# Performance work log

Hardware: AMD Instinct MI355X
Metric: run time of the kernel (lower is better)

## Reference

```python
import jax, jax.numpy as jnp
import numpy as np
import math

B, T, C, H = 2, 1024, 1024, 16
D = C // H


def setup_inputs() -> dict:
    key = jax.random.key(0)
    ks = jax.random.split(key, 7)
    scale = 1.0 / math.sqrt(C)
    q = jax.random.normal(ks[0], (B, T, C), dtype=jnp.float32)
    k = jax.random.normal(ks[1], (B, T, C), dtype=jnp.float32)
    v = jax.random.normal(ks[2], (B, T, C), dtype=jnp.float32)
    # causal mask, True = masked out (matches create_causal_mask)
    mask = jnp.triu(jnp.ones((T, T), dtype=bool), k=1)[None, None]
    Wk = jax.random.normal(ks[3], (C, C), dtype=jnp.float32) * scale
    bk = jax.random.normal(ks[4], (C,), dtype=jnp.float32) * scale
    Wc = jax.random.normal(ks[5], (C, C), dtype=jnp.float32) * scale
    bc = jax.random.normal(ks[6], (C,), dtype=jnp.float32) * scale
    return {"q": q, "k": k, "v": v, "mask": mask, "Wk": Wk, "bk": bk, "Wc": Wc, "bc": bc}


def reference(q, k, v, mask, Wk, bk, Wc, bc):
    # NOTE: original module uses self.k_attn for ALL of q, k, v (q_attn/v_attn unused).
    qB, qT, qC = q.shape
    kT = k.shape[1]
    qp = (q @ Wk.T + bk).reshape(qB, qT, H, D).transpose(0, 2, 1, 3)  # [B,H,Tq,D]
    kp = (k @ Wk.T + bk).reshape(qB, kT, H, D).transpose(0, 2, 1, 3)  # [B,H,Tk,D]
    vp = (v @ Wk.T + bk).reshape(qB, kT, H, D).transpose(0, 2, 1, 3)  # [B,H,Tk,D]
    att = jnp.einsum('bhqd,bhkd->bhqk', qp, kp) * (1.0 / math.sqrt(D))
    att = jnp.where(mask, -jnp.inf, att)
    att = jax.nn.softmax(att, axis=-1)
    y = jnp.einsum('bhqk,bhkd->bhqd', att, vp)
    y = y.transpose(0, 2, 1, 3).reshape(qB, qT, qC)
    return y @ Wc.T + bc
```

## Files before the change

### kernel.cpp

```cpp
#include <hip/hip_runtime.h>

#define T_DIM 1024
#define C_DIM 1024
#define H_DIM 16
#define D_DIM 64
#define KD    1024

typedef short  short8  __attribute__((ext_vector_type(8)));
typedef short  short4v __attribute__((ext_vector_type(4)));
typedef float  f32x4   __attribute__((ext_vector_type(4)));

__device__ __forceinline__ float bf2f(short s) {
  return __uint_as_float(((unsigned)(unsigned short)s) << 16);
}
__device__ __forceinline__ short f2bf(float f) {
  unsigned u = __float_as_uint(f);
  u += 0x7fffu + ((u >> 16) & 1u);
  return (short)(u >> 16);
}
__device__ __forceinline__ unsigned pk2(float lo, float hi) {
  return ((unsigned)(unsigned short)f2bf(lo)) | (((unsigned)(unsigned short)f2bf(hi)) << 16);
}

__device__ __forceinline__ short8 ldfrag(const void* p, size_t off, int isf32) {
  if (isf32) {
    const float* q = (const float*)p + off;
    f32x4 lo = *(const f32x4*)q;
    f32x4 hi = *(const f32x4*)(q + 4);
    short8 r;
#pragma unroll
    for (int j = 0; j < 4; ++j) { r[j] = f2bf(lo[j]); r[j + 4] = f2bf(hi[j]); }
    return r;
  }
  return *(const short8*)((const short*)p + off);
}
__device__ __forceinline__ float ldbias(const void* b, int i, int isf32) {
  return isf32 ? ((const float*)b)[i] : bf2f(((const short*)b)[i]);
}

__device__ __forceinline__ int detect_f32_inblock(const unsigned* w, int lane) {
  int c = 0;
#pragma unroll
  for (int i = 0; i < 4; ++i) {
    unsigned e = (w[lane * 4 + i] >> 7) & 0xffu;
    c += (e >= 110u && e <= 135u) ? 1 : 0;
  }
#pragma unroll
  for (int off = 32; off; off >>= 1) c += __shfl_xor(c, off);
  return (c < 128) ? 1 : 0;
}

#define SZE  ((size_t)2 * T_DIM * C_DIM)
#define QN   ((size_t)2097152)
#define WN   ((size_t)1048576)
#define BN   ((size_t)1024)
#define CVT_TOT (3 * QN + 2 * WN + 2 * BN)

__global__ __launch_bounds__(256) void cvt_k(const void* __restrict__ q,
                                             const void* __restrict__ k,
                                             const void* __restrict__ v,
                                             const void* __restrict__ wk,
                                             const void* __restrict__ wc,
                                             const void* __restrict__ bk,
                                             const void* __restrict__ bc,
                                             short* __restrict__ dst)
{
  const int lane = threadIdx.x & 63;
  const int f = detect_f32_inblock((const unsigned*)q, lane);

  const size_t idx = (size_t)blockIdx.x * 1024 + threadIdx.x * 4;
  if (idx >= CVT_TOT) return;
  const void* src;
  size_t loc;
  if      (idx <     QN)          { src = q;  loc = idx; }
  else if (idx < 2 * QN)          { src = k;  loc = idx - QN; }
  else if (idx < 3 * QN)          { src = v;  loc = idx - 2 * QN; }
  else if (idx < 3 * QN + WN)     { src = wk; loc = idx - 3 * QN; }
  else if (idx < 3 * QN + 2 * WN) { src = wc; loc = idx - 3 * QN - WN; }
  else if (idx < 3 * QN + 2 * WN + BN) { src = bk; loc = idx - 3 * QN - 2 * WN; }
  else                            { src = bc; loc = idx - 3 * QN - 2 * WN - BN; }

  short4v o;
  if (f) {
    f32x4 x = *(const f32x4*)((const float*)src + loc);
#pragma unroll
    for (int j = 0; j < 4; ++j) o[j] = f2bf(x[j]);
  } else {
    o = *(const short4v*)((const short*)src + loc);
  }
  *(short4v*)(dst + idx) = o;
}

#define LDSP 40

template<int KIND>
__global__ __launch_bounds__(256) void gemm2_k(const void* __restrict__ X0,
                                               const void* __restrict__ X1,
                                               const void* __restrict__ X2,
                                               const void* __restrict__ Wv,
                                               const void* __restrict__ Bv,
                                               void* __restrict__ outv)
{
  const int tid  = threadIdx.x;
  const int lane = tid & 63;
  const int wave = tid >> 6;
  const int col16 = lane & 15;
  const int quad  = lane >> 4;
  const int wm = wave & 1;
  const int wn = wave >> 1;

  const int f  = detect_f32_inblock((const unsigned*)Wv, lane);
  const int wf = f;
  const int xf = (KIND == 1) ? f : 0;

  const int m0 = blockIdx.x * 64;
  const int c0 = blockIdx.y * 64;

  const void* Xv = X0;
  int arow = m0;
  bool isv = false;
  short* outb = (short*)outv;
  if (KIND == 1) {
    const int src = m0 >> 11;
    Xv = (src == 0) ? X0 : (src == 1) ? X1 : X2;
    arow = m0 & 2047;
    isv = (src == 2);
    outb = (short*)outv + (size_t)src * SZE;
  }

  __shared__ short As[64 * LDSP];
  __shared__ short Bs[64 * LDSP];

  const int srow = tid >> 2;
  const int sc8  = tid & 3;

  f32x4 acc[2][2] = {};

  for (int k0 = 0; k0 < KD; k0 += 32) {
    short8 va = ldfrag(Xv, (size_t)(arow + srow) * KD + k0 + sc8 * 8, xf);
    short8 vb = ldfrag(Wv, (size_t)(c0 + srow) * KD + k0 + sc8 * 8, wf);
    if (k0) __syncthreads();
    *(short8*)&As[srow * LDSP + sc8 * 8] = va;
    *(short8*)&Bs[srow * LDSP + sc8 * 8] = vb;
    __syncthreads();

    short8 fx[2], fw[2];
#pragma unroll
    for (int i = 0; i < 2; ++i)
      fx[i] = *(const short8*)&As[(wm * 32 + i * 16 + col16) * LDSP + quad * 8];
#pragma unroll
    for (int j = 0; j < 2; ++j)
      fw[j] = *(const short8*)&Bs[(wn * 32 + j * 16 + col16) * LDSP + quad * 8];

    if (KIND == 1 && isv) {
#pragma unroll
      for (int i = 0; i < 2; ++i)
#pragma unroll
        for (int j = 0; j < 2; ++j)
          acc[i][j] = __builtin_amdgcn_mfma_f32_16x16x32_bf16(fx[i], fw[j], acc[i][j], 0, 0, 0);
    } else {
#pragma unroll
      for (int i = 0; i < 2; ++i)
#pragma unroll
        for (int j = 0; j < 2; ++j)
          acc[i][j] = __builtin_amdgcn_mfma_f32_16x16x32_bf16(fw[j], fx[i], acc[i][j], 0, 0, 0);
    }
  }

  if (KIND == 1 && isv) {
#pragma unroll
    for (int i = 0; i < 2; ++i) {
#pragma unroll
      for (int j = 0; j < 2; ++j) {
        const int c  = c0 + wn * 32 + j * 16 + col16;
        const int t0 = arow + wm * 32 + i * 16 + quad * 4;
        const float bv = ldbias(Bv, c, wf);
        short4v pk;
#pragma unroll
        for (int r = 0; r < 4; ++r) pk[r] = f2bf(acc[i][j][r] + bv);
        const int bb = t0 >> 10, t = t0 & 1023, h = c >> 6, d = c & 63;
        size_t off = (size_t)((bb * H_DIM + h) * D_DIM + d) * T_DIM + t;
        *(short4v*)(outb + off) = pk;
      }
    }
  } else {
#pragma unroll
    for (int i = 0; i < 2; ++i) {
#pragma unroll
      for (int j = 0; j < 2; ++j) {
        const int m  = arow + wm * 32 + i * 16 + col16;
        const int cb = c0 + wn * 32 + j * 16 + quad * 4;
        if (KIND == 0) {
          f32x4 pv;
#pragma unroll
          for (int r = 0; r < 4; ++r) pv[r] = acc[i][j][r] + ldbias(Bv, cb + r, wf);
          *(f32x4*)((float*)outv + (size_t)m * C_DIM + cb) = pv;
        } else {
          short4v pk;
#pragma unroll
          for (int r = 0; r < 4; ++r) pk[r] = f2bf(acc[i][j][r] + ldbias(Bv, cb + r, wf));
          const int bb = m >> 10, t = m & 1023, h = cb >> 6, d = cb & 63;
          size_t off = ((size_t)(bb * H_DIM + h) << 16) + (size_t)t * D_DIM + d;
          *(short4v*)(outb + off) = pk;
        }
      }
    }
  }
}

__global__ __launch_bounds__(256) void attn_k3(const short* __restrict__ qp,
                                               const short* __restrict__ kp,
                                               const short* __restrict__ vpt,
                                               short* __restrict__ y)
{
  const int lane = threadIdx.x & 63;
  const int wave = threadIdx.x >> 6;
  const int col  = lane & 15;
  const int quad = lane >> 4;
  const int bh = blockIdx.x;
  const int b = bh >> 4, h = bh & 15;
  const int qt = 63 - (int)blockIdx.y;
  const int q0 = qt * 16;
  const int myq = q0 + col;

  const short* qph = qp  + (size_t)bh * (T_DIM * D_DIM);
  const short* kph = kp  + (size_t)bh * (T_DIM * D_DIM);
  const short* vph = vpt + (size_t)bh * (D_DIM * T_DIM);

  const int nkt  = (q0 + 47) >> 5;
  const int base = nkt >> 2, rem = nkt & 3;
  const int cnt   = base + (wave < rem ? 1 : 0);
  const int start = wave * base + (wave < rem ? wave : rem);

  short8 bQ[2];
#pragma unroll
  for (int kk = 0; kk < 2; ++kk)
    bQ[kk] = *(const short8*)(qph + (size_t)(q0 + col) * D_DIM + kk * 32 + quad * 8);

  f32x4 O[4] = {};
  float rs = 0.0f;

  const int slA = col + ((quad & 1) * 32);
  const int slB = slA + 16;

  for (int kt = start; kt < start + cnt; ++kt) {
    const int kb = kt * 32;
    f32x4 st[2];
#pragma unroll
    for (int jt = 0; jt < 2; ++jt) {
      f32x4 s = {0.f, 0.f, 0.f, 0.f};
      const short* kbase = kph + (size_t)(kb + jt * 16 + col) * D_DIM + quad * 8;
      short8 aK0 = *(const short8*)(kbase);
      short8 aK1 = *(const short8*)(kbase + 32);
      s = __builtin_amdgcn_mfma_f32_16x16x32_bf16(aK0, bQ[0], s, 0, 0, 0);
      s = __builtin_amdgcn_mfma_f32_16x16x32_bf16(aK1, bQ[1], s, 0, 0, 0);
      st[jt] = s;
    }
#pragma unroll
    for (int jt = 0; jt < 2; ++jt) {
#pragma unroll
      for (int r = 0; r < 4; ++r) {
        const int key = kb + jt * 16 + quad * 4 + r;
        float p = __expf(st[jt][r] * 0.125f);
        p = (key > myq) ? 0.0f : p;
        st[jt][r] = p;
        rs += p;
      }
    }

    const int a0 = (int)pk2(st[0][0], st[0][1]);
    const int a1 = (int)pk2(st[0][2], st[0][3]);
    const int b0 = (int)pk2(st[1][0], st[1][1]);
    const int b1 = (int)pk2(st[1][2], st[1][3]);
    const int tA0 = __shfl(a0, slA, 64), tB0 = __shfl(b0, slA, 64);
    const int tA1 = __shfl(a1, slA, 64), tB1 = __shfl(b1, slA, 64);
    const int tA2 = __shfl(a0, slB, 64), tB2 = __shfl(b0, slB, 64);
    const int tA3 = __shfl(a1, slB, 64), tB3 = __shfl(b1, slB, 64);
    union { unsigned u[4]; short8 s8; } uu;
    uu.u[0] = (unsigned)((quad < 2) ? tA0 : tB0);
    uu.u[1] = (unsigned)((quad < 2) ? tA1 : tB1);
    uu.u[2] = (unsigned)((quad < 2) ? tA2 : tB2);
    uu.u[3] = (unsigned)((quad < 2) ? tA3 : tB3);
    const short8 bP32 = uu.s8;

#pragma unroll
    for (int dt = 0; dt < 4; ++dt) {
      short8 aV = *(const short8*)(vph + (size_t)(dt * 16 + col) * T_DIM + kb + quad * 8);
      O[dt] = __builtin_amdgcn_mfma_f32_16x16x32_bf16(aV, bP32, O[dt], 0, 0, 0);
    }
  }

  rs += __shfl_xor(rs, 16);
  rs += __shfl_xor(rs, 32);

  __shared__ float Om[4 * 4 * 16 * 16];
  __shared__ float Ll[4][16];

#pragma unroll
  for (int dt = 0; dt < 4; ++dt)
    *(f32x4*)&Om[(((wave * 4 + dt) * 16) + col) * 16 + quad * 4] = O[dt];
  if (quad == 0) Ll[wave][col] = rs;
  __syncthreads();

  float L = Ll[0][col] + Ll[1][col] + Ll[2][col] + Ll[3][col];
  f32x4 oacc = {0.f, 0.f, 0.f, 0.f};
#pragma unroll
  for (int w = 0; w < 4; ++w) {
    f32x4 ov = *(const f32x4*)&Om[(((w * 4 + wave) * 16) + col) * 16 + quad * 4];
#pragma unroll
    for (int r = 0; r < 4; ++r) oacc[r] += ov[r];
  }
  const float rl = 1.0f / L;
  const int t = q0 + col;
  const size_t ybase = ((size_t)(b * T_DIM + t)) * C_DIM + h * D_DIM + quad * 4;
  short4v pk;
#pragma unroll
  for (int r = 0; r < 4; ++r) pk[r] = f2bf(oacc[r] * rl);
  *(short4v*)(y + ybase + wave * 16) = pk;
}

extern "C" void kernel_launch(void* const* d_in, const int* in_sizes, int n_in,
                              void* d_out, int out_size, void* d_ws, size_t ws_size,
                              hipStream_t stream) {
  const void* q = d_in[0];
  const void* k = d_in[1];
  const void* v = d_in[2];
  int wi = (n_in >= 8 && in_sizes[4] == C_DIM * C_DIM) ? 4 : 3;
  const void* Wk = d_in[wi];
  const void* bk = d_in[wi + 1];
  const void* Wc = d_in[wi + 2];
  const void* bc = d_in[wi + 3];

  short* ws  = (short*)d_ws;
  short* qp  = ws;
  short* kp  = ws + SZE;
  short* vpt = ws + 2 * SZE;
  short* y   = ws + 3 * SZE;

  short* ext = ws + 4 * SZE;
  const size_t needed = (4 * SZE + CVT_TOT) * sizeof(short);
  const bool pre = (ws_size >= needed);

  dim3 blk(256);
  const void *gq = q, *gk = k, *gv = v, *gwk = Wk, *gbk = bk, *gwc = Wc, *gbc = bc;
  if (pre) {
    cvt_k<<<dim3((unsigned)((CVT_TOT + 1023) / 1024)), blk, 0, stream>>>(
        q, k, v, Wk, Wc, bk, bc, ext);
    gq  = ext;
    gk  = ext + QN;
    gv  = ext + 2 * QN;
    gwk = ext + 3 * QN;
    gwc = ext + 3 * QN + WN;
    gbk = ext + 3 * QN + 2 * WN;
    gbc = ext + 3 * QN + 2 * WN + BN;
  }

  gemm2_k<1><<<dim3(96, 16), blk, 0, stream>>>(gq, gk, gv, gwk, gbk, qp);
  attn_k3<<<dim3(32, 64), blk, 0, stream>>>(qp, kp, vpt, y);
  gemm2_k<0><<<dim3(32, 16), blk, 0, stream>>>(y, nullptr, nullptr, gwc, gbc, d_out);
}
```

Measured before the change: 179.3 us.

## Add bf16 GEMM kernels using direct global-to-LDS loads with swizzled layout

Adds new QKV-projection and output-projection GEMM kernels for the pre-converted bf16 path. They stage tiles with global_load_lds 16-byte direct loads into an XOR-swizzled LDS layout and read fragments for 16x16x32 bf16 MFMA. The QKV kernel uses 128x64 tiles, half the grid of the previous 96-block launch. The aim is to cut register staging and LDS bank conflicts in the projections, but the loop is single-buffered with two barriers per k-step, so there is no load/compute overlap.

New measurement: 169.8 us. 5.3% less time.

```diff
diff --git a/kernel.cpp b/kernel.cpp
--- a/kernel.cpp
+++ b/kernel.cpp
@@ -20,6 +20,13 @@
 }
 __device__ __forceinline__ unsigned pk2(float lo, float hi) {
   return ((unsigned)(unsigned short)f2bf(lo)) | (((unsigned)(unsigned short)f2bf(hi)) << 16);
+}
+
+__device__ __forceinline__ void gl2lds16(const short* g, short* l) {
+  __builtin_amdgcn_global_load_lds(
+      (const __attribute__((address_space(1))) unsigned int*)(const void*)g,
+      (__attribute__((address_space(3))) unsigned int*)(void*)l,
+      16, 0, 0);
 }
 
 __device__ __forceinline__ short8 ldfrag(const void* p, size_t off, int isf32) {
@@ -89,6 +96,171 @@
     o = *(const short4v*)((const short*)src + loc);
   }
   *(short4v*)(dst + idx) = o;
+}
+
+__device__ __forceinline__ void stage16(const short* gsrc, short* S, int R0,
+                                        int lane, int koff) {
+  const int rw = R0 + (lane >> 2);
+  const int q  = (lane & 3) ^ ((rw >> 1) & 3);
+  gl2lds16(gsrc + (size_t)rw * KD + koff + q * 8, &S[R0 * 32]);
+}
+__device__ __forceinline__ short8 fragread(const short* S, int row, int quad) {
+  const int sl = (row << 2) + (quad ^ ((row >> 1) & 3));
+  return *(const short8*)&S[sl << 3];
+}
+
+__global__ __launch_bounds__(256) void gemm_qkv_a(const short* __restrict__ X0,
+                                                  const short* __restrict__ X1,
+                                                  const short* __restrict__ X2,
+                                                  const short* __restrict__ Wv,
+                                                  const short* __restrict__ Bv,
+                                                  short* __restrict__ outv)
+{
+  const int tid  = threadIdx.x;
+  const int lane = tid & 63;
+  const int wave = tid >> 6;
+  const int col16 = lane & 15;
+  const int quad  = lane >> 4;
+
+  const int m0 = blockIdx.x * 128;
+  const int c0 = blockIdx.y * 64;
+
+  const int src = m0 >> 11;
+  const short* Xv = (src == 0) ? X0 : (src == 1) ? X1 : X2;
+  const int arow = m0 & 2047;
+  const bool isv = (src == 2);
+  short* outb = outv + (size_t)src * SZE;
+
+  __shared__ short As[128 * 32];
+  __shared__ short Bs[64 * 32];
+
+  const short* Xg = Xv + (size_t)arow * KD;
+  const short* Wg = Wv + (size_t)c0 * KD;
+
+  f32x4 acc[2][4] = {};
+
+  for (int k0 = 0; k0 < KD; k0 += 32) {
+    if (k0) __syncthreads();
+    stage16(Xg, As, wave * 32,      lane, k0);
+    stage16(Xg, As, wave * 32 + 16, lane, k0);
+    stage16(Wg, Bs, wave * 16,      lane, k0);
+    __syncthreads();
+
+    short8 fx[2], fw[4];
+#pragma unroll
+    for (int i = 0; i < 2; ++i)
+      fx[i] = fragread(As, wave * 32 + i * 16 + col16, quad);
+#pragma unroll
+    for (int j = 0; j < 4; ++j)
+      fw[j] = fragread(Bs, j * 16 + col16, quad);
+
+    if (isv) {
+#pragma unroll
+      for (int i = 0; i < 2; ++i)
+#pragma unroll
+        for (int j = 0; j < 4; ++j)
+          acc[i][j] = __builtin_amdgcn_mfma_f32_16x16x32_bf16(fx[i], fw[j], acc[i][j], 0, 0, 0);
+    } else {
+#pragma unroll
+      for (int i = 0; i < 2; ++i)
+#pragma unroll
+        for (int j = 0; j < 4; ++j)
+          acc[i][j] = __builtin_amdgcn_mfma_f32_16x16x32_bf16(fw[j], fx[i], acc[i][j], 0, 0, 0);
+    }
+  }
+
+  if (isv) {
+#pragma unroll
+    for (int i = 0; i < 2; ++i) {
+#pragma unroll
+      for (int j = 0; j < 4; ++j) {
+        const int c  = c0 + j * 16 + col16;
+        const int t0 = arow + wave * 32 + i * 16 + quad * 4;
+        const float bv = bf2f(Bv[c]);
+        short4v pk;
+#pragma unroll
+        for (int r = 0; r < 4; ++r) pk[r] = f2bf(acc[i][j][r] + bv);
+        const int bb = t0 >> 10, t = t0 & 1023, h = c >> 6, d = c & 63;
+        size_t off = (size_t)((bb * H_DIM + h) * D_DIM + d) * T_DIM + t;
+        *(short4v*)(outb + off) = pk;
+      }
+    }
+  } else {
+#pragma unroll
+    for (int i = 0; i < 2; ++i) {
+#pragma unroll
+      for (int j = 0; j < 4; ++j) {
+        const int m  = arow + wave * 32 + i * 16 + col16;
+        const int cb = c0 + j * 16 + quad * 4;
+        short4v bv4 = *(const short4v*)(Bv + cb);
+        short4v pk;
+#pragma unroll
+        for (int r = 0; r < 4; ++r) pk[r] = f2bf(acc[i][j][r] + bf2f(bv4[r]));
+        const int bb = m >> 10, t = m & 1023, h = cb >> 6, d = cb & 63;
+        size_t off = ((size_t)(bb * H_DIM + h) << 16) + (size_t)t * D_DIM + d;
+        *(short4v*)(outb + off) = pk;
+      }
+    }
+  }
+}
+
+__global__ __launch_bounds__(256) void gemm_out_a(const short* __restrict__ Xb,
+                                                  const short* __restrict__ Wv,
+                                                  const short* __restrict__ Bv,
+                                                  float* __restrict__ outv)
+{
+  const int tid  = threadIdx.x;
+  const int lane = tid & 63;
+  const int wave = tid >> 6;
+  const int col16 = lane & 15;
+  const int quad  = lane >> 4;
+  const int wm = wave & 1;
+  const int wn = wave >> 1;
+
+  const int m0 = blockIdx.x * 64;
+  const int c0 = blockIdx.y * 64;
+
+  __shared__ short As[64 * 32];
+  __shared__ short Bs[64 * 32];
+
+  const short* Xg = Xb + (size_t)m0 * KD;
+  const short* Wg = Wv + (size_t)c0 * KD;
+
+  f32x4 acc[2][2] = {};
+
+  for (int k0 = 0; k0 < KD; k0 += 32) {
+    if (k0) __syncthreads();
+    stage16(Xg, As, wave * 16, lane, k0);
+    stage16(Wg, Bs, wave * 16, lane, k0);
+    __syncthreads();
+
+    short8 fx[2], fw[2];
+#pragma unroll
+    for (int i = 0; i < 2; ++i)
+      fx[i] = fragread(As, wm * 32 + i * 16 + col16, quad);
+#pragma unroll
+    for (int j = 0; j < 2; ++j)
+      fw[j] = fragread(Bs, wn * 32 + j * 16 + col16, quad);
+
+#pragma unroll
+    for (int i = 0; i < 2; ++i)
+#pragma unroll
+      for (int j = 0; j < 2; ++j)
+        acc[i][j] = __builtin_amdgcn_mfma_f32_16x16x32_bf16(fw[j], fx[i], acc[i][j], 0, 0, 0);
+  }
+
+#pragma unroll
+  for (int i = 0; i < 2; ++i) {
+#pragma unroll
+    for (int j = 0; j < 2; ++j) {
+      const int m  = m0 + wm * 32 + i * 16 + col16;
+      const int cb = c0 + wn * 32 + j * 16 + quad * 4;
+      f32x4 pv;
+#pragma unroll
+      for (int r = 0; r < 4; ++r) pv[r] = acc[i][j][r] + bf2f(Bv[cb + r]);
+      *(f32x4*)(outv + (size_t)m * C_DIM + cb) = pv;
+    }
+  }
 }
 
 #define LDSP 40
@@ -342,20 +514,23 @@
   const bool pre = (ws_size >= needed);
 
   dim3 blk(256);
-  const void *gq = q, *gk = k, *gv = v, *gwk = Wk, *gbk = bk, *gwc = Wc, *gbc = bc;
   if (pre) {
     cvt_k<<<dim3((unsigned)((CVT_TOT + 1023) / 1024)), blk, 0, stream>>>(
         q, k, v, Wk, Wc, bk, bc, ext);
-    gq  = ext;
-    gk  = ext + QN;
-    gv  = ext + 2 * QN;
-    gwk = ext + 3 * QN;
-    gwc = ext + 3 * QN + WN;
-    gbk = ext + 3 * QN + 2 * WN;
-    gbc = ext + 3 * QN + 2 * WN + BN;
-  }
-
-  gemm2_k<1><<<dim3(96, 16), blk, 0, stream>>>(gq, gk, gv, gwk, gbk, qp);
-  attn_k3<<<dim3(32, 64), blk, 0, stream>>>(qp, kp, vpt, y);
-  gemm2_k<0><<<dim3(32, 16), blk, 0, stream>>>(y, nullptr, nullptr, gwc, gbc, d_out);
-}
+    const short* gq  = ext;
+    const short* gk  = ext + QN;
+    const short* gv  = ext + 2 * QN;
+    const short* gwk = ext + 3 * QN;
+    const short* gwc = ext + 3 * QN + WN;
+    const short* gbk = ext + 3 * QN + 2 * WN;
+    const short* gbc = ext + 3 * QN + 2 * WN + BN;
+
+    gemm_qkv_a<<<dim3(48, 16), blk, 0, stream>>>(gq, gk, gv, gwk, gbk, qp);
+    attn_k3<<<dim3(32, 64), blk, 0, stream>>>(qp, kp, vpt, y);
+    gemm_out_a<<<dim3(32, 16), blk, 0, stream>>>(y, gwc, gbc, (float*)d_out);
+  } else {
+    gemm2_k<1><<<dim3(96, 16), blk, 0, stream>>>(q, k, v, Wk, bk, qp);
+    attn_k3<<<dim3(32, 64), blk, 0, stream>>>(qp, kp, vpt, y);
+    gemm2_k<0><<<dim3(32, 16), blk, 0, stream>>>(y, nullptr, nullptr, Wc, bc, d_out);
+  }
+}
```
